# Performance work log

Hardware: AMD Instinct MI355X
Metric: run time of the kernel (lower is better)

## Reference

```python
import jax, jax.numpy as jnp
import numpy as np

VAR0, VAR1 = 0.1, 0.2
THRESH = 0.5
NEG_POS = 3
NEG_INF = -1e30


def point_form(b):
    # (cx,cy,w,h) -> (x1,y1,x2,y2)
    return jnp.concatenate([b[..., :2] - b[..., 2:] * 0.5,
                            b[..., :2] + b[..., 2:] * 0.5], -1)


def iou(a, b):
    # a: [G,4], b: [A,4], both xyxy -> [G,A]
    tl = jnp.maximum(a[:, None, :2], b[None, :, :2])
    br = jnp.minimum(a[:, None, 2:], b[None, :, 2:])
    wh = jnp.clip(br - tl, 0.0)
    inter = wh[..., 0] * wh[..., 1]
    area_a = (a[:, 2] - a[:, 0]) * (a[:, 3] - a[:, 1])
    area_b = (b[:, 2] - b[:, 0]) * (b[:, 3] - b[:, 1])
    return inter / (area_a[:, None] + area_b[None, :] - inter)


def encode_single(gt_boxes, gt_labels, anchors):
    # gt_boxes [G,4] xyxy, gt_labels [G], anchors [A,4] cxcywh
    ov = iou(gt_boxes, point_form(anchors))            # [G,A]
    best_prior_idx = jnp.argmax(ov, axis=1)            # [G] guaranteed match
    best_truth_ov = jnp.max(ov, axis=0)                # [A]
    best_truth_idx = jnp.argmax(ov, axis=0)            # [A]
    G = gt_boxes.shape[0]
    best_truth_ov = best_truth_ov.at[best_prior_idx].set(2.0)
    best_truth_idx = best_truth_idx.at[best_prior_idx].set(jnp.arange(G))
    matches = gt_boxes[best_truth_idx]                 # [A,4]
    conf = jnp.where(best_truth_ov < THRESH, 0, gt_labels[best_truth_idx] + 1)
    m_cxcy = (matches[:, :2] + matches[:, 2:]) * 0.5
    m_wh = matches[:, 2:] - matches[:, :2]
    g_cxcy = (m_cxcy - anchors[:, :2]) / (VAR0 * anchors[:, 2:])
    g_wh = jnp.log(m_wh / anchors[:, 2:]) / VAR1
    return conf, jnp.concatenate([g_cxcy, g_wh], -1)


def smooth_l1(d):
    ad = jnp.abs(d)
    return jnp.where(ad < 1.0, 0.5 * d * d, ad - 0.5)


def ssd_guarantee_loss(pred_conf, pred_loc, anchors_b, gt_boxes, gt_labels):
    # anchors_b: per-image anchors [B,A,4] (cxcywh)
    conf_t, loc_t = jax.vmap(encode_single)(gt_boxes, gt_labels, anchors_b)
    loc_t = jax.lax.stop_gradient(loc_t)               # loc_t.detach() in torch
    pos = conf_t > 0                                   # [B,A]
    N = jnp.sum(pos).astype(pred_loc.dtype)
    loc_loss = jnp.sum(jnp.where(pos[..., None], smooth_l1(pred_loc - loc_t), 0.0))
    logp = jax.nn.log_softmax(pred_conf, axis=-1)
    ce = -jnp.take_along_axis(logp, conf_t[..., None], axis=-1)[..., 0]  # [B,A]
    A = pred_conf.shape[1]
    pos_num = jnp.sum(pos, axis=1)                     # [B]
    neg_num = jnp.maximum(10, jnp.minimum(pos_num * NEG_POS, A - pos_num))
    neg_ce = jnp.where(conf_t == 0, ce, NEG_INF)
    neg_sorted = -jnp.sort(-neg_ce, axis=1)            # descending hard-negative sort
    rank = jnp.arange(A)
    take = (rank[None, :] < neg_num[:, None]) & (neg_sorted > 0.5 * NEG_INF)
    class_loss = (jnp.sum(jnp.where(pos, ce, 0.0))
                  + jnp.sum(jnp.where(take, neg_sorted, 0.0))) / N
    return class_loss, loc_loss / N, N


def decode(loc, anchors):
    # loc [B,A,4], anchors [A,4] cxcywh -> refined anchors [B,A,4] cxcywh
    cxcy = anchors[None, :, :2] + loc[..., :2] * VAR0 * anchors[None, :, 2:]
    wh = anchors[None, :, 2:] * jnp.exp(loc[..., 2:] * VAR1)
    return jnp.concatenate([cxcy, wh], -1)


def setup_inputs() -> dict:
    key = jax.random.key(0)
    ks = jax.random.split(key, 10)
    B, A, C, G = 32, 16320, 81, 32
    objectness = jax.random.normal(ks[0], (B, A, 2), jnp.float32)
    refine_loc = 0.1 * jax.random.normal(ks[1], (B, A, 4), jnp.float32)
    pred_conf = jax.random.normal(ks[2], (B, A, C), jnp.float32)
    pred_loc = 0.1 * jax.random.normal(ks[3], (B, A, 4), jnp.float32)
    # anchors: valid normalized cxcywh
    a_cxcy = 0.05 + 0.9 * jax.random.uniform(ks[4], (1, A, 2), jnp.float32)
    a_wh = 0.02 + 0.23 * jax.random.uniform(ks[5], (1, A, 2), jnp.float32)
    anchors = jnp.concatenate([a_cxcy, a_wh], -1)
    # gt boxes: valid xyxy in [0,1]
    g_cxcy = 0.2 + 0.6 * jax.random.uniform(ks[6], (B, G, 2), jnp.float32)
    g_wh = 0.05 + 0.25 * jax.random.uniform(ks[7], (B, G, 2), jnp.float32)
    gt_boxes = jnp.clip(jnp.concatenate([g_cxcy - g_wh * 0.5, g_cxcy + g_wh * 0.5], -1), 0.0, 1.0)
    gt_labels = jax.random.randint(ks[8], (B, G), 0, C - 1, jnp.int32)
    return {"objectness": objectness, "refine_loc": refine_loc, "pred_conf": pred_conf,
            "pred_loc": pred_loc, "anchors": anchors, "gt_boxes": gt_boxes,
            "gt_labels": gt_labels}


def reference(objectness, refine_loc, pred_conf, pred_loc, anchors, gt_boxes, gt_labels):
    a0 = anchors[0]                                    # [A,4]
    B = pred_conf.shape[0]
    anchors_b = jnp.broadcast_to(a0, (B,) + a0.shape)
    # ARM: binary objectness, labels zeroed
    arm_cls, arm_loc, _ = ssd_guarantee_loss(objectness, refine_loc, anchors_b,
                                             gt_boxes, jnp.zeros_like(gt_labels))
    # ODM: match against per-image refined anchors
    refined = decode(refine_loc, a0)
    odm_cls, odm_loc, _ = ssd_guarantee_loss(pred_conf, pred_loc, refined,
                                             gt_boxes, gt_labels)
    total = arm_cls + arm_loc + odm_cls + odm_loc
    return (total, odm_cls, odm_loc, arm_cls, arm_loc)
```

## Files before the change

kernel.cpp:

```cpp
#include <hip/hip_runtime.h>
#include <hip/hip_bf16.h>

constexpr int NB = 32;
constexpr int NA = 16320;
constexpr int NG = 32;
constexpr int NC = 81;
constexpr int ODM_GRID = 2048;

__device__ __forceinline__ float sl1(float d) {
    float ad = fabsf(d);
    return ad < 1.f ? 0.5f * d * d : ad - 0.5f;
}

__device__ __forceinline__ unsigned long long umax64(unsigned long long a, unsigned long long b) {
    return a > b ? a : b;
}

__global__ __launch_bounds__(256) void k_match(
    const float* __restrict__ anchors,
    const float* __restrict__ refine_loc,
    const float* __restrict__ gt_boxes,
    float* __restrict__ ws_ov,
    unsigned char* __restrict__ ws_idx,
    unsigned long long* __restrict__ ws_part)
{
    int row = blockIdx.x >> 6;
    int chunk = blockIdx.x & 63;
    int lossId = row >> 5, b = row & 31;
    int tid = threadIdx.x;
    __shared__ float4 s_gt[NG];
    __shared__ float s_ga[NG];
    __shared__ unsigned long long s_part[4][NG];
    if (tid < NG) {
        float4 g = *(const float4*)&gt_boxes[(size_t)(b * NG + tid) * 4];
        s_gt[tid] = g;
        s_ga[tid] = (g.z - g.x) * (g.w - g.y);
    }
    __syncthreads();
    int a = chunk * 256 + tid;
    bool valid = a < NA;
    int al = valid ? a : NA - 1;
    float4 an = *(const float4*)&anchors[(size_t)al * 4];
    float acx = an.x, acy = an.y, aw = an.z, ah = an.w;
    if (lossId) {
        float4 rl = *(const float4*)&refine_loc[((size_t)b * NA + al) * 4];
        acx += rl.x * 0.1f * aw;
        acy += rl.y * 0.1f * ah;
        aw *= __expf(rl.z * 0.2f);
        ah *= __expf(rl.w * 0.2f);
    }
    float ax1 = acx - aw * 0.5f, ay1 = acy - ah * 0.5f;
    float ax2 = acx + aw * 0.5f, ay2 = acy + ah * 0.5f;
    float aarea = (ax2 - ax1) * (ay2 - ay1);

    float ovg[NG];
    float best = -1.f; int bg = 0;
    #pragma unroll
    for (int g = 0; g < NG; g++) {
        float4 G = s_gt[g];
        float tlx = fmaxf(G.x, ax1);
        float tly = fmaxf(G.y, ay1);
        float brx = fminf(G.z, ax2);
        float bry = fminf(G.w, ay2);
        float w = brx - tlx; w = w > 0.f ? w : 0.f;
        float h = bry - tly; h = h > 0.f ? h : 0.f;
        float inter = w * h;
        float uni = s_ga[g] + aarea - inter;
        float ov = inter * __builtin_amdgcn_rcpf(uni);
        if (!valid) ov = 0.f;
        ovg[g] = ov;
        if (ov > best) { best = ov; bg = g; }
    }
    if (valid) {
        size_t sec = (size_t)row * NA;
        ws_ov[sec + a] = best;
        ws_idx[sec + a] = (unsigned char)bg;
    }
    int lane = tid & 63, wv = tid >> 6;
    #pragma unroll
    for (int g = 0; g < NG; g++) {
        float m = ovg[g];
        m = fmaxf(m, __shfl_xor(m, 1));
        m = fmaxf(m, __shfl_xor(m, 2));
        m = fmaxf(m, __shfl_xor(m, 4));
        m = fmaxf(m, __shfl_xor(m, 8));
        m = fmaxf(m, __shfl_xor(m, 16));
        m = fmaxf(m, __shfl_xor(m, 32));
        unsigned long long ball = __ballot(ovg[g] == m);
        int first = __ffsll((long long)ball) - 1;
        if (lane == 0) {
            unsigned aw_ = (unsigned)(chunk * 256 + wv * 64 + first);
            s_part[wv][g] = ((unsigned long long)__float_as_uint(m) << 32)
                            | (0xFFFFFFFFu - aw_);
        }
    }
    __syncthreads();
    if (tid < NG) {
        unsigned long long k = s_part[0][tid];
        #pragma unroll
        for (int i = 1; i < 4; i++) k = umax64(k, s_part[i][tid]);
        ws_part[(size_t)blockIdx.x * NG + tid] = k;
    }
}

__global__ __launch_bounds__(256) void k_conf(
    const int* __restrict__ gt_labels,
    const unsigned long long* __restrict__ ws_part,
    const float* __restrict__ ws_ov,
    const unsigned char* __restrict__ ws_idx,
    const float* __restrict__ objectness,
    const float* __restrict__ anchors,
    const float* __restrict__ gt_boxes,
    const float* __restrict__ arm_pred,
    int* __restrict__ match,
    float* __restrict__ negce,
    int* __restrict__ pos_cnt,
    float2* __restrict__ pConf)
{
    int row = blockIdx.x >> 3;
    int chunk = blockIdx.x & 7;
    int lossId = row >> 5, b = row & 31;
    int tid = threadIdx.x;
    __shared__ int s_oa[NG];
    __shared__ int s_lab[NG];
    __shared__ float4 s_gt[NG];
    __shared__ unsigned s_mask[512];
    __shared__ unsigned long long s_pp[8][NG];
    for (int i = tid; i < 512; i += 256) s_mask[i] = 0u;
    {
        int g = tid & 31, s = tid >> 5;
        unsigned long long k = 0ull;
        for (int c = s; c < 64; c += 8)
            k = umax64(k, ws_part[(size_t)(row * 64 + c) * NG + g]);
        s_pp[s][g] = k;
    }
    __syncthreads();
    if (tid < NG) {
        unsigned long long k = s_pp[0][tid];
        #pragma unroll
        for (int i = 1; i < 8; i++) k = umax64(k, s_pp[i][tid]);
        unsigned a = 0xFFFFFFFFu - (unsigned)(k & 0xFFFFFFFFull);
        s_oa[tid] = (int)a;
        s_lab[tid] = lossId ? gt_labels[b * NG + tid] : 0;
        s_gt[tid] = *(const float4*)&gt_boxes[(size_t)(b * NG + tid) * 4];
        atomicOr(&s_mask[a >> 5], 1u << (a & 31));
    }
    __syncthreads();
    size_t sec = (size_t)row * NA;
    int base = chunk * 2040;
    int cnt = 0;
    float pce = 0.f, ploc = 0.f;
    for (int a = base + tid; a < base + 2040; a += 256) {
        float ov = ws_ov[sec + a];
        int g = ws_idx[sec + a];
        if (s_mask[a >> 5] & (1u << (a & 31))) {
            for (int j = NG - 1; j >= 0; j--)
                if (s_oa[j] == a) { g = j; ov = 2.0f; break; }
        }
        int conf = (ov < 0.5f) ? 0 : (s_lab[g] + 1);
        cnt += (conf > 0);
        if (lossId) {
            match[sec + a] = conf | (g << 16);
        } else {
            size_t idx = sec + a;
            float2 x = *(const float2*)&objectness[idx * 2];
            float mx = fmaxf(x.x, x.y);
            float lse = mx + __logf(__expf(x.x - mx) + __expf(x.y - mx));
            float ce = lse - (conf ? x.y : x.x);
            if (conf > 0) {
                pce += ce;
                negce[idx] = 0.f;
                float4 an = *(const float4*)&anchors[(size_t)a * 4];
                float4 G = s_gt[g];
                float mcx = (G.x + G.z) * 0.5f, mcy = (G.y + G.w) * 0.5f;
                float mw = G.z - G.x, mh = G.w - G.y;
                float t0 = (mcx - an.x) / (0.1f * an.z);
                float t1 = (mcy - an.y) / (0.1f * an.w);
                float t2 = __logf(mw / an.z) / 0.2f;
                float t3 = __logf(mh / an.w) / 0.2f;
                float4 pl = *(const float4*)&arm_pred[idx * 4];
                ploc += sl1(pl.x - t0) + sl1(pl.y - t1) + sl1(pl.z - t2) + sl1(pl.w - t3);
            } else {
                negce[idx] = ce;
            }
        }
    }
    #pragma unroll
    for (int o = 32; o > 0; o >>= 1) {
        cnt += __shfl_down(cnt, o);
        pce += __shfl_down(pce, o);
        ploc += __shfl_down(ploc, o);
    }
    __shared__ int s_c[4];
    __shared__ float s_p0[4], s_p1[4];
    if ((tid & 63) == 0) {
        int w = tid >> 6;
        s_c[w] = cnt; s_p0[w] = pce; s_p1[w] = ploc;
    }
    __syncthreads();
    if (tid == 0) {
        pos_cnt[blockIdx.x] = s_c[0] + s_c[1] + s_c[2] + s_c[3];
        pConf[blockIdx.x] = make_float2(s_p0[0] + s_p0[1] + s_p0[2] + s_p0[3],
                                        s_p1[0] + s_p1[1] + s_p1[2] + s_p1[3]);
    }
}

__device__ __forceinline__ void block_reduce2_store(float v0, float v1, float2* dst) {
    #pragma unroll
    for (int o = 32; o > 0; o >>= 1) { v0 += __shfl_down(v0, o); v1 += __shfl_down(v1, o); }
    __shared__ float s0[4], s1[4];
    int w = threadIdx.x >> 6;
    if ((threadIdx.x & 63) == 0) { s0[w] = v0; s1[w] = v1; }
    __syncthreads();
    if (threadIdx.x == 0) {
        float t0 = 0.f, t1 = 0.f;
        #pragma unroll
        for (int i = 0; i < 4; i++) { t0 += s0[i]; t1 += s1[i]; }
        *dst = make_float2(t0, t1);
    }
}

__device__ __forceinline__ void odm_anchor(
    int idx, const float* x, float x80, int m, int sub,
    const float* __restrict__ anchors, const float* __restrict__ refine_loc,
    const float* __restrict__ gt_boxes, const float* __restrict__ pred_loc,
    float* __restrict__ negce, float& pce, float& ploc)
{
    int conf = m & 0xFFFF; int g = m >> 16;
    float mx = x80;
    #pragma unroll
    for (int j = 0; j < 10; j++) mx = fmaxf(mx, x[j]);
    mx = fmaxf(mx, __shfl_xor(mx, 1));
    mx = fmaxf(mx, __shfl_xor(mx, 2));
    mx = fmaxf(mx, __shfl_xor(mx, 4));
    float s = (sub == 0) ? __expf(x80 - mx) : 0.f;
    float sel = (sub == 0 && conf == 80) ? x80 : 0.f;
    #pragma unroll
    for (int j = 0; j < 10; j++) {
        s += __expf(x[j] - mx);
        sel += (sub + 8 * j == conf) ? x[j] : 0.f;
    }
    s += __shfl_xor(s, 1);   sel += __shfl_xor(sel, 1);
    s += __shfl_xor(s, 2);   sel += __shfl_xor(sel, 2);
    s += __shfl_xor(s, 4);   sel += __shfl_xor(sel, 4);
    float ce = mx + __logf(s) - sel;
    if (sub == 0) {
        if (conf > 0) {
            pce += ce;
            negce[idx] = 0.f;
            int b = idx / NA, a = idx - b * NA;
            float4 an = *(const float4*)&anchors[(size_t)a * 4];
            float4 rl = *(const float4*)&refine_loc[(size_t)idx * 4];
            float acx = an.x + rl.x * 0.1f * an.z;
            float acy = an.y + rl.y * 0.1f * an.w;
            float aw = an.z * __expf(rl.z * 0.2f);
            float ah = an.w * __expf(rl.w * 0.2f);
            const float* gb = &gt_boxes[(size_t)(b * NG + g) * 4];
            float mcx = (gb[0] + gb[2]) * 0.5f, mcy = (gb[1] + gb[3]) * 0.5f;
            float mw = gb[2] - gb[0], mh = gb[3] - gb[1];
            float t0 = (mcx - acx) / (0.1f * aw);
            float t1 = (mcy - acy) / (0.1f * ah);
            float t2 = __logf(mw / aw) / 0.2f;
            float t3 = __logf(mh / ah) / 0.2f;
            float4 pl = *(const float4*)&pred_loc[(size_t)idx * 4];
            ploc += sl1(pl.x - t0) + sl1(pl.y - t1) + sl1(pl.z - t2) + sl1(pl.w - t3);
        } else {
            negce[idx] = ce;
        }
    }
}

__global__ __launch_bounds__(256, 4) void k_odm_loss(
    const float* __restrict__ pred_conf,
    const float* __restrict__ pred_loc,
    const float* __restrict__ anchors,
    const float* __restrict__ refine_loc,
    const float* __restrict__ gt_boxes,
    const int* __restrict__ match,
    float* __restrict__ negce,
    float2* __restrict__ partial)
{
    int lane = threadIdx.x & 63;
    int sub = lane & 7;
    int grp = lane >> 3;
    int wid = blockIdx.x * 4 + (threadIdx.x >> 6);
    const int NWAVE = ODM_GRID * 4;
    const int TOT = NB * NA / 8;
    float pce = 0.f, ploc = 0.f;

    float x[10], x80; int m, idx;
    {
        idx = wid * 8 + grp;
        const float* p = pred_conf + (size_t)idx * NC;
        #pragma unroll
        for (int j = 0; j < 10; j++) x[j] = p[sub + 8 * j];
        x80 = (sub == 0) ? p[80] : -3.0e38f;
        m = match[idx];
    }
    for (int gi = wid; gi < TOT; gi += NWAVE) {
        float y[10], y80 = 0.f; int my = 0, idxy = 0;
        int nx = gi + NWAVE;
        if (nx < TOT) {
            idxy = nx * 8 + grp;
            const float* p = pred_conf + (size_t)idxy * NC;
            #pragma unroll
            for (int j = 0; j < 10; j++) y[j] = p[sub + 8 * j];
            y80 = (sub == 0) ? p[80] : -3.0e38f;
            my = match[idxy];
        }
        odm_anchor(idx, x, x80, m, sub, anchors, refine_loc, gt_boxes, pred_loc,
                   negce, pce, ploc);
        #pragma unroll
        for (int j = 0; j < 10; j++) x[j] = y[j];
        x80 = y80; m = my; idx = idxy;
    }
    block_reduce2_store(pce, ploc, &partial[blockIdx.x]);
}

__global__ __launch_bounds__(256) void k_topk(
    const float* __restrict__ negce,
    const int* __restrict__ pos_cnt,
    float* __restrict__ topk)
{
    int blk = blockIdx.x;
    int tid = threadIdx.x;
    size_t sec = (size_t)blk * NA;
    float v[64];
    #pragma unroll
    for (int q = 0; q < 64; q++) {
        int i = tid + (q << 8);
        v[q] = (i < NA) ? negce[sec + i] : 0.f;
    }
    __shared__ int s_red[4];
    __shared__ float s_redf[4];
    int p = 0;
    #pragma unroll
    for (int j = 0; j < 8; j++) p += pos_cnt[blk * 8 + j];
    int k = p * 3; if (k > NA - p) k = NA - p; if (k < 10) k = 10;

    unsigned lo = 0u, hi = 0x7F800000u;
    while (lo < hi) {
        unsigned mid = (lo + hi) >> 1;
        float fmid = __uint_as_float(mid);
        int c = 0;
        #pragma unroll
        for (int q = 0; q < 64; q++) c += (v[q] > fmid);
        #pragma unroll
        for (int o = 32; o > 0; o >>= 1) c += __shfl_down(c, o);
        if ((tid & 63) == 0) s_red[tid >> 6] = c;
        __syncthreads();
        int total = s_red[0] + s_red[1] + s_red[2] + s_red[3];
        __syncthreads();
        if (total < k) hi = mid; else lo = mid + 1;
    }
    float V = __uint_as_float(lo);
    int c = 0; float sum = 0.f;
    #pragma unroll
    for (int q = 0; q < 64; q++) {
        if (v[q] > V) { c++; sum += v[q]; }
    }
    #pragma unroll
    for (int o = 32; o > 0; o >>= 1) { c += __shfl_down(c, o); sum += __shfl_down(sum, o); }
    if ((tid & 63) == 0) { s_red[tid >> 6] = c; s_redf[tid >> 6] = sum; }
    __syncthreads();
    if (tid == 0) {
        int cg = s_red[0] + s_red[1] + s_red[2] + s_red[3];
        float sg = s_redf[0] + s_redf[1] + s_redf[2] + s_redf[3];
        topk[blk] = sg + (float)(k - cg) * V;
    }
}

__global__ __launch_bounds__(256) void k_final(
    const float2* __restrict__ pConf, const float2* __restrict__ pOdm,
    const int* __restrict__ pos_cnt, const float* __restrict__ topk,
    float* __restrict__ out)
{
    int tid = threadIdx.x;
    float a0 = 0.f, a1 = 0.f, o0 = 0.f, o1 = 0.f;
    for (int i = tid; i < 512; i += 256) { float2 v = pConf[i]; a0 += v.x; a1 += v.y; }
    for (int i = tid; i < ODM_GRID; i += 256) { float2 v = pOdm[i]; o0 += v.x; o1 += v.y; }
    float n0 = (float)pos_cnt[tid];
    float n1 = (float)pos_cnt[256 + tid];
    float t0 = (tid < NB) ? topk[tid] : 0.f;
    float t1 = (tid < NB) ? topk[NB + tid] : 0.f;
    #pragma unroll
    for (int o = 32; o > 0; o >>= 1) {
        a0 += __shfl_down(a0, o); a1 += __shfl_down(a1, o);
        o0 += __shfl_down(o0, o); o1 += __shfl_down(o1, o);
        n0 += __shfl_down(n0, o); n1 += __shfl_down(n1, o);
        t0 += __shfl_down(t0, o); t1 += __shfl_down(t1, o);
    }
    __shared__ float s[4][8];
    if ((tid & 63) == 0) {
        int w = tid >> 6;
        s[w][0] = a0; s[w][1] = a1; s[w][2] = o0; s[w][3] = o1;
        s[w][4] = n0; s[w][5] = n1; s[w][6] = t0; s[w][7] = t1;
    }
    __syncthreads();
    if (tid == 0) {
        float armce = 0.f, armloc = 0.f, odmce = 0.f, odmloc = 0.f;
        float N0 = 0.f, N1 = 0.f, tk0 = 0.f, tk1 = 0.f;
        #pragma unroll
        for (int i = 0; i < 4; i++) {
            armce += s[i][0]; armloc += s[i][1]; odmce += s[i][2]; odmloc += s[i][3];
            N0 += s[i][4]; N1 += s[i][5]; tk0 += s[i][6]; tk1 += s[i][7];
        }
        float cls0 = (armce + tk0) / N0, loc0 = armloc / N0;
        float cls1 = (odmce + tk1) / N1, loc1 = odmloc / N1;
        out[0] = cls0 + loc0 + cls1 + loc1;
        out[1] = cls1;
        out[2] = loc1;
        out[3] = cls0;
        out[4] = loc0;
    }
}

extern "C" void kernel_launch(void* const* d_in, const int* in_sizes, int n_in,
                              void* d_out, int out_size, void* d_ws, size_t ws_size,
                              hipStream_t stream) {
    const float* objectness = (const float*)d_in[0];
    const float* refine_loc = (const float*)d_in[1];
    const float* pred_conf  = (const float*)d_in[2];
    const float* pred_loc   = (const float*)d_in[3];
    const float* anchors    = (const float*)d_in[4];
    const float* gt_boxes   = (const float*)d_in[5];
    const int*   gt_labels  = (const int*)d_in[6];

    char* w = (char*)d_ws;
    size_t off = 0;
    int* pos_cnt = (int*)(w + off); off += 512 * sizeof(int);
    float* topk = (float*)(w + off); off += 64 * sizeof(float);
    off = (off + 15) & ~(size_t)15;
    float2* pConf = (float2*)(w + off); off += 512 * 8;
    float2* pOdm = (float2*)(w + off); off += (size_t)ODM_GRID * 8;
    unsigned long long* ws_part = (unsigned long long*)(w + off);
    off += (size_t)64 * 64 * NG * 8;
    off = (off + 15) & ~(size_t)15;
    float* ws_ov = (float*)(w + off); off += (size_t)2 * NB * NA * 4;
    unsigned char* ws_idx = (unsigned char*)(w + off); off += (size_t)2 * NB * NA;
    off = (off + 15) & ~(size_t)15;
    int* match = (int*)(w + off); off += (size_t)2 * NB * NA * 4;
    float* negce = (float*)(w + off); off += (size_t)2 * NB * NA * 4;

    k_match<<<64 * 64, 256, 0, stream>>>(anchors, refine_loc, gt_boxes,
                                         ws_ov, ws_idx, ws_part);
    k_conf<<<64 * 8, 256, 0, stream>>>(gt_labels, ws_part, ws_ov, ws_idx,
                                       objectness, anchors, gt_boxes, refine_loc,
                                       match, negce, pos_cnt, pConf);
    k_odm_loss<<<ODM_GRID, 256, 0, stream>>>(pred_conf, pred_loc, anchors, refine_loc,
                                             gt_boxes, match + (size_t)NB * NA,
                                             negce + (size_t)NB * NA, pOdm);
    k_topk<<<2 * NB, 256, 0, stream>>>(negce, pos_cnt, topk);
    k_final<<<1, 256, 0, stream>>>(pConf, pOdm, pos_cnt, topk, (float*)d_out);
}
```

Measured before the change: 134.4 us.

## Remap ODM loss to half-wave per anchor and widen top-k blocks

The ODM loss kernel now handles each anchor's 81 logits with 32 lanes, two anchors per wavefront, instead of 8 lanes per anchor with 10 strided loads each. The goal is contiguous, coalesced row loads and fewer serial exp/compare steps per lane, at the cost of more shuffle rounds and more iterations per wave. The top-k kernel moves to 512 threads per block with 32 registers per thread instead of 64, which lowers register pressure and adds parallelism to the binary-search counting. The occupancy hint on the loss kernel is also dropped.

```diff
diff --git a/kernel.cpp b/kernel.cpp
--- a/kernel.cpp
+++ b/kernel.cpp
@@ -220,57 +220,7 @@
     }
 }
 
-__device__ __forceinline__ void odm_anchor(
-    int idx, const float* x, float x80, int m, int sub,
-    const float* __restrict__ anchors, const float* __restrict__ refine_loc,
-    const float* __restrict__ gt_boxes, const float* __restrict__ pred_loc,
-    float* __restrict__ negce, float& pce, float& ploc)
-{
-    int conf = m & 0xFFFF; int g = m >> 16;
-    float mx = x80;
-    #pragma unroll
-    for (int j = 0; j < 10; j++) mx = fmaxf(mx, x[j]);
-    mx = fmaxf(mx, __shfl_xor(mx, 1));
-    mx = fmaxf(mx, __shfl_xor(mx, 2));
-    mx = fmaxf(mx, __shfl_xor(mx, 4));
-    float s = (sub == 0) ? __expf(x80 - mx) : 0.f;
-    float sel = (sub == 0 && conf == 80) ? x80 : 0.f;
-    #pragma unroll
-    for (int j = 0; j < 10; j++) {
-        s += __expf(x[j] - mx);
-        sel += (sub + 8 * j == conf) ? x[j] : 0.f;
-    }
-    s += __shfl_xor(s, 1);   sel += __shfl_xor(sel, 1);
-    s += __shfl_xor(s, 2);   sel += __shfl_xor(sel, 2);
-    s += __shfl_xor(s, 4);   sel += __shfl_xor(sel, 4);
-    float ce = mx + __logf(s) - sel;
-    if (sub == 0) {
-        if (conf > 0) {
-            pce += ce;
-            negce[idx] = 0.f;
-            int b = idx / NA, a = idx - b * NA;
-            float4 an = *(const float4*)&anchors[(size_t)a * 4];
-            float4 rl = *(const float4*)&refine_loc[(size_t)idx * 4];
-            float acx = an.x + rl.x * 0.1f * an.z;
-            float acy = an.y + rl.y * 0.1f * an.w;
-            float aw = an.z * __expf(rl.z * 0.2f);
-            float ah = an.w * __expf(rl.w * 0.2f);
-            const float* gb = &gt_boxes[(size_t)(b * NG + g) * 4];
-            float mcx = (gb[0] + gb[2]) * 0.5f, mcy = (gb[1] + gb[3]) * 0.5f;
-            float mw = gb[2] - gb[0], mh = gb[3] - gb[1];
-            float t0 = (mcx - acx) / (0.1f * aw);
-            float t1 = (mcy - acy) / (0.1f * ah);
-            float t2 = __logf(mw / aw) / 0.2f;
-            float t3 = __logf(mh / ah) / 0.2f;
-            float4 pl = *(const float4*)&pred_loc[(size_t)idx * 4];
-            ploc += sl1(pl.x - t0) + sl1(pl.y - t1) + sl1(pl.z - t2) + sl1(pl.w - t3);
-        } else {
-            negce[idx] = ce;
-        }
-    }
-}
-
-__global__ __launch_bounds__(256, 4) void k_odm_loss(
+__global__ __launch_bounds__(256) void k_odm_loss(
     const float* __restrict__ pred_conf,
     const float* __restrict__ pred_loc,
     const float* __restrict__ anchors,
@@ -281,43 +231,77 @@
     float2* __restrict__ partial)
 {
     int lane = threadIdx.x & 63;
-    int sub = lane & 7;
-    int grp = lane >> 3;
+    int half = lane >> 5;
+    int t = lane & 31;
     int wid = blockIdx.x * 4 + (threadIdx.x >> 6);
     const int NWAVE = ODM_GRID * 4;
-    const int TOT = NB * NA / 8;
+    const int TOT = NB * NA / 2;
     float pce = 0.f, ploc = 0.f;
 
-    float x[10], x80; int m, idx;
+    float x0, x1, x2; int m, idx;
     {
-        idx = wid * 8 + grp;
+        idx = wid * 2 + half;
         const float* p = pred_conf + (size_t)idx * NC;
-        #pragma unroll
-        for (int j = 0; j < 10; j++) x[j] = p[sub + 8 * j];
-        x80 = (sub == 0) ? p[80] : -3.0e38f;
+        x0 = p[t];
+        x1 = p[32 + t];
+        x2 = (t < 17) ? p[64 + t] : -3.0e38f;
         m = match[idx];
     }
-    for (int gi = wid; gi < TOT; gi += NWAVE) {
-        float y[10], y80 = 0.f; int my = 0, idxy = 0;
-        int nx = gi + NWAVE;
-        if (nx < TOT) {
-            idxy = nx * 8 + grp;
-            const float* p = pred_conf + (size_t)idxy * NC;
-            #pragma unroll
-            for (int j = 0; j < 10; j++) y[j] = p[sub + 8 * j];
-            y80 = (sub == 0) ? p[80] : -3.0e38f;
+    for (int pi = wid; pi < TOT; pi += NWAVE) {
+        float y0 = 0.f, y1 = 0.f, y2 = -3.0e38f; int my = 0, idxy = 0;
+        int np = pi + NWAVE;
+        if (np < TOT) {
+            idxy = np * 2 + half;
+            const float* q = pred_conf + (size_t)idxy * NC;
+            y0 = q[t];
+            y1 = q[32 + t];
+            y2 = (t < 17) ? q[64 + t] : -3.0e38f;
             my = match[idxy];
         }
-        odm_anchor(idx, x, x80, m, sub, anchors, refine_loc, gt_boxes, pred_loc,
-                   negce, pce, ploc);
-        #pragma unroll
-        for (int j = 0; j < 10; j++) x[j] = y[j];
-        x80 = y80; m = my; idx = idxy;
+        int conf = m & 0xFFFF; int g = m >> 16;
+        float mx = fmaxf(fmaxf(x0, x1), x2);
+        #pragma unroll
+        for (int o = 1; o <= 16; o <<= 1) mx = fmaxf(mx, __shfl_xor(mx, o));
+        float s = __expf(x0 - mx) + __expf(x1 - mx) + ((t < 17) ? __expf(x2 - mx) : 0.f);
+        float sel = (conf == t) ? x0 : 0.f;
+        sel += (conf == 32 + t) ? x1 : 0.f;
+        sel += (t < 17 && conf == 64 + t) ? x2 : 0.f;
+        #pragma unroll
+        for (int o = 1; o <= 16; o <<= 1) {
+            s += __shfl_xor(s, o);
+            sel += __shfl_xor(sel, o);
+        }
+        float ce = mx + __logf(s) - sel;
+        if (t == 0) {
+            if (conf > 0) {
+                pce += ce;
+                negce[idx] = 0.f;
+                int b = idx / NA, a = idx - b * NA;
+                float4 an = *(const float4*)&anchors[(size_t)a * 4];
+                float4 rl = *(const float4*)&refine_loc[(size_t)idx * 4];
+                float acx = an.x + rl.x * 0.1f * an.z;
+                float acy = an.y + rl.y * 0.1f * an.w;
+                float aw = an.z * __expf(rl.z * 0.2f);
+                float ah = an.w * __expf(rl.w * 0.2f);
+                const float* gb = &gt_boxes[(size_t)(b * NG + g) * 4];
+                float mcx = (gb[0] + gb[2]) * 0.5f, mcy = (gb[1] + gb[3]) * 0.5f;
+                float mw = gb[2] - gb[0], mh = gb[3] - gb[1];
+                float t0 = (mcx - acx) / (0.1f * aw);
+                float t1 = (mcy - acy) / (0.1f * ah);
+                float t2 = __logf(mw / aw) / 0.2f;
+                float t3 = __logf(mh / ah) / 0.2f;
+                float4 pl = *(const float4*)&pred_loc[(size_t)idx * 4];
+                ploc += sl1(pl.x - t0) + sl1(pl.y - t1) + sl1(pl.z - t2) + sl1(pl.w - t3);
+            } else {
+                negce[idx] = ce;
+            }
+        }
+        x0 = y0; x1 = y1; x2 = y2; m = my; idx = idxy;
     }
     block_reduce2_store(pce, ploc, &partial[blockIdx.x]);
 }
 
-__global__ __launch_bounds__(256) void k_topk(
+__global__ __launch_bounds__(512) void k_topk(
     const float* __restrict__ negce,
     const int* __restrict__ pos_cnt,
     float* __restrict__ topk)
@@ -325,14 +309,14 @@
     int blk = blockIdx.x;
     int tid = threadIdx.x;
     size_t sec = (size_t)blk * NA;
-    float v[64];
-    #pragma unroll
-    for (int q = 0; q < 64; q++) {
-        int i = tid + (q << 8);
+    float v[32];
+    #pragma unroll
+    for (int q = 0; q < 32; q++) {
+        int i = tid + (q << 9);
         v[q] = (i < NA) ? negce[sec + i] : 0.f;
     }
-    __shared__ int s_red[4];
-    __shared__ float s_redf[4];
+    __shared__ int s_red[8];
+    __shared__ float s_redf[8];
     int p = 0;
     #pragma unroll
     for (int j = 0; j < 8; j++) p += pos_cnt[blk * 8 + j];
@@ -344,19 +328,21 @@
         float fmid = __uint_as_float(mid);
         int c = 0;
         #pragma unroll
-        for (int q = 0; q < 64; q++) c += (v[q] > fmid);
+        for (int q = 0; q < 32; q++) c += (v[q] > fmid);
         #pragma unroll
         for (int o = 32; o > 0; o >>= 1) c += __shfl_down(c, o);
         if ((tid & 63) == 0) s_red[tid >> 6] = c;
         __syncthreads();
-        int total = s_red[0] + s_red[1] + s_red[2] + s_red[3];
+        int total = 0;
+        #pragma unroll
+        for (int j = 0; j < 8; j++) total += s_red[j];
         __syncthreads();
         if (total < k) hi = mid; else lo = mid + 1;
     }
     float V = __uint_as_float(lo);
     int c = 0; float sum = 0.f;
     #pragma unroll
-    for (int q = 0; q < 64; q++) {
+    for (int q = 0; q < 32; q++) {
         if (v[q] > V) { c++; sum += v[q]; }
     }
     #pragma unroll
@@ -364,8 +350,9 @@
     if ((tid & 63) == 0) { s_red[tid >> 6] = c; s_redf[tid >> 6] = sum; }
     __syncthreads();
     if (tid == 0) {
-        int cg = s_red[0] + s_red[1] + s_red[2] + s_red[3];
-        float sg = s_redf[0] + s_redf[1] + s_redf[2] + s_redf[3];
+        int cg = 0; float sg = 0.f;
+        #pragma unroll
+        for (int j = 0; j < 8; j++) { cg += s_red[j]; sg += s_redf[j]; }
         topk[blk] = sg + (float)(k - cg) * V;
     }
 }
@@ -450,6 +437,6 @@
     k_odm_loss<<<ODM_GRID, 256, 0, stream>>>(pred_conf, pred_loc, anchors, refine_loc,
                                              gt_boxes, match + (size_t)NB * NA,
                                              negce + (size_t)NB * NA, pOdm);
-    k_topk<<<2 * NB, 256, 0, stream>>>(negce, pos_cnt, topk);
+    k_topk<<<2 * NB, 512, 0, stream>>>(negce, pos_cnt, topk);
     k_final<<<1, 256, 0, stream>>>(pConf, pOdm, pos_cnt, topk, (float*)d_out);
 }
```

Result: slower. 151.6 us (+12.9%).
